# Kernel tuning notes

Hardware: AMD Instinct MI355X
Metric: run time of the kernel (lower is better)

## Reference

```python
import jax, jax.numpy as jnp
import numpy as np

HEAD_DIM = 128
NUM_Q_HEAD = 32
NUM_KV_HEAD = 8
GROUP_SIZE = 128
EPS = 1e-5
WINDOW = 512
CAP = 50.0
CLIP_L, CLIP_R = -0.01, 1.01
SCALE = 1.0 / np.sqrt(HEAD_DIM)
NEG = -1e9


def group_rmsnorm(x, gamma, gsz, eps):
    # x: [B, S, H]; per-group RMS over contiguous chunks of size gsz, then learned scale
    b, s, h = x.shape
    xg = x.reshape(b, s, h // gsz, gsz)
    rms = jnp.sqrt(jnp.mean(xg * xg, axis=-1, keepdims=True) + eps)
    return (xg / rms).reshape(b, s, h) * gamma


def setup_inputs() -> dict:
    key = jax.random.key(0)
    k1, k2, k3, k4, k5 = jax.random.split(key, 5)
    B, S = 2, 2048
    q = jax.random.normal(k1, (B, S, NUM_Q_HEAD, HEAD_DIM), dtype=jnp.float32)
    k = jax.random.normal(k2, (B, S, NUM_KV_HEAD, HEAD_DIM), dtype=jnp.float32)
    v = jax.random.normal(k3, (B, S, NUM_KV_HEAD, HEAD_DIM), dtype=jnp.float32)
    # GroupRMSNorm weights ~ U(init_range) = U(-1, 1)
    gamma_q = jax.random.uniform(k4, (NUM_Q_HEAD * HEAD_DIM,), dtype=jnp.float32, minval=-1.0, maxval=1.0)
    gamma_k = jax.random.uniform(k5, (NUM_KV_HEAD * HEAD_DIM,), dtype=jnp.float32, minval=-1.0, maxval=1.0)
    return {"q": q, "k": k, "v": v, "gamma_q": gamma_q, "gamma_k": gamma_k}


def reference(q, k, v, gamma_q, gamma_k):
    B, Sq, Hq, D = q.shape
    Sk, Hkv = k.shape[1], k.shape[2]
    # QK GroupRMSNorm on flattened hidden dim
    qn = group_rmsnorm(q.reshape(B, Sq, Hq * D), gamma_q, GROUP_SIZE, EPS).reshape(B, Sq, Hq, D)
    kn = group_rmsnorm(k.reshape(B, Sk, Hkv * D), gamma_k, GROUP_SIZE, EPS).reshape(B, Sk, Hkv, D)
    # GQA: repeat_interleave kv heads to match q heads
    rep = Hq // Hkv
    kr = jnp.repeat(kn, rep, axis=2)
    vr = jnp.repeat(v, rep, axis=2)
    # scores: [B, H, Sq, Sk]
    logits = jnp.einsum('bqhd,bkhd->bhqk', qn, kr) * SCALE
    # softmax capping (temperature path skipped when cap is set)
    logits = jnp.tanh(logits / CAP) * CAP
    # causal + sliding-window mask (aligned at sequence end)
    i = jnp.arange(Sq)[:, None]
    j = jnp.arange(Sk)[None, :]
    pos = i + (Sk - Sq)
    allowed = (j <= pos) & (pos - j <= WINDOW)
    logits = jnp.where(allowed, logits, NEG)
    probs = jax.nn.softmax(logits.astype(jnp.float32), axis=-1)
    # softmax clipping: clamp(probs * (r - l) + l, 0, 1)
    probs = jnp.clip(probs * (CLIP_R - CLIP_L) + CLIP_L, 0.0, 1.0)
    # output: [B, Sq, H, D]
    o = jnp.einsum('bhqk,bkhd->bqhd', probs.astype(q.dtype), vr)
    return o
```

## Files before the change

### kernel.cpp

```cpp
#include <hip/hip_runtime.h>

#define SEQ     2048
#define NQH     32
#define NKV     8
#define HD      128
#define WINDOW  512
#define QT      64
#define EPS_F   1e-5f
#define CQ2     0.12752981793f
#define PSTR    72

#define KN_OFF  0ull
#define VT_OFF  8388608ull

#define ROWPAT(r, hg) ((((r) & 3) + 8 * ((r) >> 2)) + 4 * (hg))

#define ASYNC_BAR() asm volatile("s_waitcnt vmcnt(0)\n\ts_barrier" ::: "memory")
#define LGKM_BAR()  asm volatile("s_waitcnt lgkmcnt(0)\n\ts_barrier" ::: "memory")

using bf16x8 = __attribute__((ext_vector_type(8))) __bf16;
using f32x16 = __attribute__((ext_vector_type(16))) float;

__device__ __forceinline__ void dma16(const void* g, void* l) {
    __builtin_amdgcn_global_load_lds(
        (const __attribute__((address_space(1))) unsigned int*)g,
        (__attribute__((address_space(3))) unsigned int*)l, 16, 0, 0);
}

__global__ __launch_bounds__(256)
void prep(const float* __restrict__ k, const float* __restrict__ v,
          const float* __restrict__ gk,
          __bf16* __restrict__ kn, __bf16* __restrict__ vt)
{
    __shared__ __align__(16) __bf16 sT[HD * 72];
    const int blk = blockIdx.x;
    const int tid = threadIdx.x;
    if (blk < 512) {
        const int l16  = tid & 15;
        const int rsub = tid >> 4;
        #pragma unroll
        for (int it = 0; it < 4; it++) {
            const int row = blk * 64 + it * 16 + rsub;
            const float* src = k + (size_t)row * HD + l16 * 8;
            const float* g   = gk + (row & 7) * HD + l16 * 8;
            float4 a  = *(const float4*)(src);
            float4 b4 = *(const float4*)(src + 4);
            float ss = a.x*a.x + a.y*a.y + a.z*a.z + a.w*a.w
                     + b4.x*b4.x + b4.y*b4.y + b4.z*b4.z + b4.w*b4.w;
            ss += __shfl_xor(ss, 1); ss += __shfl_xor(ss, 2);
            ss += __shfl_xor(ss, 4); ss += __shfl_xor(ss, 8);
            const float rs = rsqrtf(ss * (1.f / 128.f) + EPS_F);
            float4 g0 = *(const float4*)(g);
            float4 g1 = *(const float4*)(g + 4);
            bf16x8 o;
            o[0] = (__bf16)(a.x  * rs * g0.x);  o[1] = (__bf16)(a.y  * rs * g0.y);
            o[2] = (__bf16)(a.z  * rs * g0.z);  o[3] = (__bf16)(a.w  * rs * g0.w);
            o[4] = (__bf16)(b4.x * rs * g1.x);  o[5] = (__bf16)(b4.y * rs * g1.y);
            o[6] = (__bf16)(b4.z * rs * g1.z);  o[7] = (__bf16)(b4.w * rs * g1.w);
            *(bf16x8*)(kn + (size_t)row * HD + l16 * 8) = o;
        }
    } else {
        const int blk2 = blk - 512;
        const int st  = blk2 & 31;
        const int kvh = (blk2 >> 5) & 7;
        const int b   = blk2 >> 8;
        const int s0  = st * 64;
        {
            const int r  = tid >> 2;
            const int q4 = tid & 3;
            const float* src = v + ((size_t)(b * SEQ + s0 + r) * NKV + kvh) * HD;
            #pragma unroll
            for (int u = 0; u < 8; u++) {
                const int d0 = q4 * 4 + u * 16;
                float4 x = *(const float4*)(src + d0);
                sT[(d0 + 0) * 72 + r] = (__bf16)x.x;
                sT[(d0 + 1) * 72 + r] = (__bf16)x.y;
                sT[(d0 + 2) * 72 + r] = (__bf16)x.z;
                sT[(d0 + 3) * 72 + r] = (__bf16)x.w;
            }
        }
        __syncthreads();
        {
            const int c     = tid & 7;
            const int dbase = tid >> 3;
            __bf16* dst = vt + ((size_t)(b * NKV + kvh) * HD) * SEQ + s0;
            #pragma unroll
            for (int i = 0; i < 4; i++) {
                const int d = dbase + i * 32;
                bf16x8 w = *(const bf16x8*)&sT[d * 72 + c * 8];
                *(bf16x8*)(dst + (size_t)d * SEQ + c * 8) = w;
            }
        }
    }
}

__global__ __launch_bounds__(256, 2)
void swa_main(const float* __restrict__ q, const __bf16* __restrict__ kn,
              const __bf16* __restrict__ vt, const float* __restrict__ gq,
              float* __restrict__ out)
{
    __shared__ __align__(16) __bf16 sKV[2][QT * HD];
    __shared__ __align__(16) __bf16 sP[QT * PSTR];
    __shared__ float sLp[2][QT];
    __shared__ float sInvL[QT];

    const int wg   = blockIdx.x;
    const int qt   = wg & 31;
    const int h    = (wg >> 5) & 31;
    const int b    = wg >> 10;
    const int kvh  = h >> 2;
    const int i0   = qt * QT;
    const int tid  = threadIdx.x;
    const int lane = tid & 63;
    const int wave = tid >> 6;
    const int mhalf = wave & 1;
    const int nhalf = wave >> 1;
    const int m    = lane & 31;
    const int hg   = lane >> 5;

    const char* k_src[4];  const char* v_src[4];
    int kq_off[4];  int v_off[4];
    {
        const char* kn_head = (const char*)kn + ((size_t)b * SEQ * NKV + kvh) * 256;
        const char* vt_head = (const char*)vt + ((size_t)(b * NKV + kvh) * HD) * (SEQ * 2);
        #pragma unroll
        for (int i = 0; i < 4; i++) {
            const int chunk = wave * 4 + i;
            {
                const int r    = chunk * 4 + (lane >> 4);
                const int cpos = lane & 15;
                const int c    = (cpos & 8) | ((cpos ^ r) & 7);
                k_src[i]  = kn_head + (size_t)r * (NKV * HD * 2) + c * 16;
                kq_off[i] = chunk * 1024;
            }
            {
                const int r    = chunk * 8 + (lane >> 3);
                const int cpos = lane & 7;
                const int c    = cpos ^ (r & 7);
                v_src[i] = vt_head + (size_t)r * (SEQ * 2) + c * 16;
                v_off[i] = chunk * 1024;
            }
        }
    }

    const int t_lo   = (i0 >= WINDOW ? (i0 - WINDOW) : 0) >> 6;
    const int t_hi   = i0 >> 6;
    const int ttbias = t_hi - 8;
    const int krow   = nhalf * 32 + m;

    {
        const size_t ko = (size_t)t_lo * 64 * (NKV * HD * 2);
        const int p0 = (t_lo - ttbias) & 1;
        #pragma unroll
        for (int i = 0; i < 4; i++) dma16(k_src[i] + ko, (char*)&sKV[p0][0] + kq_off[i]);
    }

    bf16x8 qf[8];
    {
        const int qrow = i0 + mhalf * 32 + m;
        const float* qp = q + ((size_t)(b * SEQ + qrow) * NQH + h) * HD;
        float4 qb[16];
        float ss = 0.0f;
        #pragma unroll
        for (int kf = 0; kf < 8; kf++) {
            const int d0 = kf * 16 + hg * 8;
            float4 a  = *(const float4*)(qp + d0);
            float4 b4 = *(const float4*)(qp + d0 + 4);
            qb[kf * 2] = a; qb[kf * 2 + 1] = b4;
            ss += a.x*a.x + a.y*a.y + a.z*a.z + a.w*a.w
                + b4.x*b4.x + b4.y*b4.y + b4.z*b4.z + b4.w*b4.w;
        }
        ss += __shfl_xor(ss, 32);
        const float rs = rsqrtf(ss * (1.f / 128.f) + EPS_F) * CQ2;
        const float* gp = gq + h * HD;
        #pragma unroll
        for (int kf = 0; kf < 8; kf++) {
            const int d0 = kf * 16 + hg * 8;
            float4 g0 = *(const float4*)(gp + d0);
            float4 g1 = *(const float4*)(gp + d0 + 4);
            bf16x8 f;
            f[0] = (__bf16)(qb[kf*2].x   * rs * g0.x);
            f[1] = (__bf16)(qb[kf*2].y   * rs * g0.y);
            f[2] = (__bf16)(qb[kf*2].z   * rs * g0.z);
            f[3] = (__bf16)(qb[kf*2].w   * rs * g0.w);
            f[4] = (__bf16)(qb[kf*2+1].x * rs * g1.x);
            f[5] = (__bf16)(qb[kf*2+1].y * rs * g1.y);
            f[6] = (__bf16)(qb[kf*2+1].z * rs * g1.z);
            f[7] = (__bf16)(qb[kf*2+1].w * rs * g1.w);
            qf[kf] = f;
        }
    }

    float lacc[16];
    #pragma unroll
    for (int i = 0; i < 16; i++) lacc[i] = 0.f;
    bf16x8 ec[9][2];

    #pragma unroll
    for (int tt = 0; tt < 9; tt++) {
        const int t = ttbias + tt;
        if (t >= t_lo) {
            ASYNC_BAR();
            const __bf16* kb = &sKV[tt & 1][0];
            bf16x8 bk[8];
            #pragma unroll
            for (int kf = 0; kf < 8; kf++) {
                const int cc  = kf * 2 + hg;
                const int pos = (cc & 8) | ((cc ^ krow) & 7);
                bk[kf] = *(const bf16x8*)(kb + krow * HD + pos * 8);
            }
            if (t < t_hi) {
                const size_t ko = (size_t)(t + 1) * 64 * (NKV * HD * 2);
                #pragma unroll
                for (int i = 0; i < 4; i++)
                    dma16(k_src[i] + ko, (char*)&sKV[(tt + 1) & 1][0] + kq_off[i]);
            }
            f32x16 c;
            #pragma unroll
            for (int i = 0; i < 16; i++) c[i] = 0.f;
            #pragma unroll
            for (int kf = 0; kf < 8; kf++)
                c = __builtin_amdgcn_mfma_f32_32x32x16_bf16(qf[kf], bk[kf], c, 0, 0, 0);

            const bool do_mask = (t == t_hi) || (t == t_lo && i0 >= WINDOW);
            const int kj = t * 64 + krow;
            float e[16];
            #pragma unroll
            for (int r = 0; r < 16; r++) {
                float ev = __builtin_amdgcn_exp2f(c[r]);
                if (do_mask) {
                    const int qi = i0 + mhalf * 32 + ROWPAT(r, hg);
                    ev = ((unsigned)(qi - kj) <= WINDOW) ? ev : 0.f;
                }
                lacc[r] += ev;
                e[r] = ev;
            }
            bf16x8 p0v, p1v;
            #pragma unroll
            for (int j = 0; j < 8; j++) { p0v[j] = (__bf16)e[j]; p1v[j] = (__bf16)e[8 + j]; }
            ec[tt][0] = p0v;  ec[tt][1] = p1v;
        }
    }

    #pragma unroll
    for (int r = 0; r < 16; r++) {
        float l = lacc[r];
        l += __shfl_xor(l, 1);  l += __shfl_xor(l, 2);  l += __shfl_xor(l, 4);
        l += __shfl_xor(l, 8);  l += __shfl_xor(l, 16);
        lacc[r] = l;
    }
    if (m == 0) {
        #pragma unroll
        for (int r = 0; r < 16; r++)
            sLp[nhalf][mhalf * 32 + ROWPAT(r, hg)] = lacc[r];
    }
    __syncthreads();
    if (tid < QT) sInvL[tid] = __builtin_amdgcn_rcpf(sLp[0][tid] + sLp[1][tid]);
    __syncthreads();

    float ar[16];
    #pragma unroll
    for (int r = 0; r < 16; r++) ar[r] = 1.02f * sInvL[mhalf * 32 + ROWPAT(r, hg)];

    {
        const size_t vo = (size_t)t_lo * 128;
        const int p0 = (t_lo - ttbias) & 1;
        #pragma unroll
        for (int i = 0; i < 4; i++) dma16(v_src[i] + vo, (char*)&sKV[p0][0] + v_off[i]);
    }

    f32x16 o0, o1;
    #pragma unroll
    for (int i = 0; i < 16; i++) { o0[i] = 0.f; o1[i] = 0.f; }

    #pragma unroll
    for (int tt = 0; tt < 9; tt++) {
        const int t = ttbias + tt;
        if (t >= t_lo) {
            ASYNC_BAR();
            #pragma unroll
            for (int half = 0; half < 2; half++) {
                #pragma unroll
                for (int j = 0; j < 8; j++) {
                    const int r = half * 8 + j;
                    const float ee = (float)ec[tt][half][j];
                    const float f = fminf(fmaxf(fmaf(ee, ar[r], -0.01f), 0.f), 1.f);
                    sP[(mhalf * 32 + ROWPAT(r, hg)) * PSTR + krow] = (__bf16)f;
                }
            }
            LGKM_BAR();
            const __bf16* vb = &sKV[tt & 1][0];
            bf16x8 pa[4], vf0[4], vf1[4];
            #pragma unroll
            for (int kf = 0; kf < 4; kf++) {
                pa[kf] = *(const bf16x8*)&sP[(mhalf * 32 + m) * PSTR + kf * 16 + hg * 8];
                const int cc = kf * 2 + hg;
                const int row0 = nhalf * 64 + m;
                const int row1 = nhalf * 64 + 32 + m;
                vf0[kf] = *(const bf16x8*)(vb + row0 * 64 + ((cc ^ row0) & 7) * 8);
                vf1[kf] = *(const bf16x8*)(vb + row1 * 64 + ((cc ^ row1) & 7) * 8);
            }
            if (t < t_hi) {
                const size_t vo = (size_t)(t + 1) * 128;
                #pragma unroll
                for (int i = 0; i < 4; i++)
                    dma16(v_src[i] + vo, (char*)&sKV[(tt + 1) & 1][0] + v_off[i]);
            }
            #pragma unroll
            for (int kf = 0; kf < 4; kf++) {
                o0 = __builtin_amdgcn_mfma_f32_32x32x16_bf16(pa[kf], vf0[kf], o0, 0, 0, 0);
                o1 = __builtin_amdgcn_mfma_f32_32x32x16_bf16(pa[kf], vf1[kf], o1, 0, 0, 0);
            }
        }
    }

    #pragma unroll
    for (int r = 0; r < 16; r++) {
        const int row = i0 + mhalf * 32 + ROWPAT(r, hg);
        float* op = out + ((size_t)(b * SEQ + row) * NQH + h) * HD + nhalf * 64 + m;
        op[0]  = o0[r];
        op[32] = o1[r];
    }
}

extern "C" void kernel_launch(void* const* d_in, const int* in_sizes, int n_in,
                              void* d_out, int out_size, void* d_ws, size_t ws_size,
                              hipStream_t stream) {
    const float* q  = (const float*)d_in[0];
    const float* k  = (const float*)d_in[1];
    const float* v  = (const float*)d_in[2];
    const float* gq = (const float*)d_in[3];
    const float* gk = (const float*)d_in[4];
    float* out = (float*)d_out;

    __bf16* kn = (__bf16*)((char*)d_ws + KN_OFF);
    __bf16* vt = (__bf16*)((char*)d_ws + VT_OFF);

    prep<<<1024, 256, 0, stream>>>(k, v, gk, kn, vt);
    swa_main<<<2 * NQH * (SEQ / QT), 256, 0, stream>>>(q, kn, vt, gq, out);
}
```

Measured before the change: 219.4 us.

## Share K/V tiles across GQA head group with register-staged prefetch

The attention kernel now processes all four query heads of a KV head in one 512-thread workgroup, so each K/V tile is loaded into LDS once and reused by four heads instead of being reloaded per head. The async global-to-LDS DMA is replaced with register-staged prefetch two tiles ahead. The second pass recomputes QK scores rather than caching exponentials in registers. Each wave now owns 32 rows across the full head dimension, which removes the cross-wave row-sum reduction through shared memory. The V transpose in prep is also reworked to use vector LDS writes. In exchange it uses more registers and LDS (64KB), duplicates the QK MFMA work, and adds extra barriers.

```diff
diff --git a/kernel.cpp b/kernel.cpp
--- a/kernel.cpp
+++ b/kernel.cpp
@@ -8,31 +8,23 @@
 #define QT      64
 #define EPS_F   1e-5f
 #define CQ2     0.12752981793f
-#define PSTR    72
 
 #define KN_OFF  0ull
 #define VT_OFF  8388608ull
 
 #define ROWPAT(r, hg) ((((r) & 3) + 8 * ((r) >> 2)) + 4 * (hg))
 
-#define ASYNC_BAR() asm volatile("s_waitcnt vmcnt(0)\n\ts_barrier" ::: "memory")
 #define LGKM_BAR()  asm volatile("s_waitcnt lgkmcnt(0)\n\ts_barrier" ::: "memory")
 
 using bf16x8 = __attribute__((ext_vector_type(8))) __bf16;
 using f32x16 = __attribute__((ext_vector_type(16))) float;
-
-__device__ __forceinline__ void dma16(const void* g, void* l) {
-    __builtin_amdgcn_global_load_lds(
-        (const __attribute__((address_space(1))) unsigned int*)g,
-        (__attribute__((address_space(3))) unsigned int*)l, 16, 0, 0);
-}
 
 __global__ __launch_bounds__(256)
 void prep(const float* __restrict__ k, const float* __restrict__ v,
           const float* __restrict__ gk,
           __bf16* __restrict__ kn, __bf16* __restrict__ vt)
 {
-    __shared__ __align__(16) __bf16 sT[HD * 72];
+    __shared__ __align__(16) __bf16 sT[64 * 136];
     const int blk = blockIdx.x;
     const int tid = threadIdx.x;
     if (blk < 512) {
@@ -66,98 +58,196 @@
         const int b   = blk2 >> 8;
         const int s0  = st * 64;
         {
-            const int r  = tid >> 2;
-            const int q4 = tid & 3;
-            const float* src = v + ((size_t)(b * SEQ + s0 + r) * NKV + kvh) * HD;
+            const int r = tid >> 2, seg = (tid & 3) * 32;
+            const float* src = v + ((size_t)(b * SEQ + s0 + r) * NKV + kvh) * HD + seg;
             #pragma unroll
-            for (int u = 0; u < 8; u++) {
-                const int d0 = q4 * 4 + u * 16;
-                float4 x = *(const float4*)(src + d0);
-                sT[(d0 + 0) * 72 + r] = (__bf16)x.x;
-                sT[(d0 + 1) * 72 + r] = (__bf16)x.y;
-                sT[(d0 + 2) * 72 + r] = (__bf16)x.z;
-                sT[(d0 + 3) * 72 + r] = (__bf16)x.w;
+            for (int u = 0; u < 4; u++) {
+                float4 x = *(const float4*)(src + u * 8);
+                float4 y = *(const float4*)(src + u * 8 + 4);
+                bf16x8 w;
+                w[0] = (__bf16)x.x; w[1] = (__bf16)x.y; w[2] = (__bf16)x.z; w[3] = (__bf16)x.w;
+                w[4] = (__bf16)y.x; w[5] = (__bf16)y.y; w[6] = (__bf16)y.z; w[7] = (__bf16)y.w;
+                *(bf16x8*)&sT[r * 136 + seg + u * 8] = w;
             }
         }
         __syncthreads();
-        {
-            const int c     = tid & 7;
-            const int dbase = tid >> 3;
-            __bf16* dst = vt + ((size_t)(b * NKV + kvh) * HD) * SEQ + s0;
+        __bf16* vtb = vt + (size_t)(b * NKV + kvh) * HD * SEQ;
+        #pragma unroll
+        for (int it = 0; it < 4; it++) {
+            const int id   = tid + it * 256;
+            const int d    = id >> 3;
+            const int sblk = id & 7;
+            bf16x8 w;
             #pragma unroll
-            for (int i = 0; i < 4; i++) {
-                const int d = dbase + i * 32;
-                bf16x8 w = *(const bf16x8*)&sT[d * 72 + c * 8];
-                *(bf16x8*)(dst + (size_t)d * SEQ + c * 8) = w;
+            for (int i = 0; i < 8; i++) {
+                const int j = i ^ sblk;
+                w[j] = sT[(sblk * 8 + j) * 136 + d];
             }
+            *(bf16x8*)(vtb + (size_t)d * SEQ + s0 + sblk * 8) = w;
         }
     }
 }
 
-__global__ __launch_bounds__(256, 2)
+
+#define L1_ITER(T, RDP, LDK0, LDK1, WK0, WK1)                                           \
+  {                                                                                     \
+    const char* kb = smem + (RDP) * 16384;                                              \
+    bf16x8 bk0[8], bk1[8];                                                              \
+    _Pragma("unroll")                                                                   \
+    for (int kf = 0; kf < 8; kf++) {                                                    \
+      const int cc = kf * 2 + hg;                                                       \
+      bk0[kf] = *(const bf16x8*)(kb + m * 256 + (((cc & 8) | ((cc ^ m) & 7)) * 16));    \
+      const int r1 = 32 + m;                                                            \
+      bk1[kf] = *(const bf16x8*)(kb + r1 * 256 + (((cc & 8) | ((cc ^ r1) & 7)) * 16));  \
+    }                                                                                   \
+    { const int tc = ((T) + 2 > t_hi) ? t_hi : (T) + 2;                                 \
+      const char* pp = kgp + (size_t)tc * 131072;                                       \
+      LDK0 = *(const int4*)pp;  LDK1 = *(const int4*)(pp + 16); }                       \
+    { char* dst = smem + (1 - (RDP)) * 16384;                                           \
+      *(int4*)(dst + kds0) = WK0;  *(int4*)(dst + kds1) = WK1; }                        \
+    f32x16 c0, c1;                                                                      \
+    _Pragma("unroll")                                                                   \
+    for (int i = 0; i < 16; i++) { c0[i] = 0.f; c1[i] = 0.f; }                          \
+    _Pragma("unroll")                                                                   \
+    for (int kf = 0; kf < 8; kf++) {                                                    \
+      c0 = __builtin_amdgcn_mfma_f32_32x32x16_bf16(qf[kf], bk0[kf], c0, 0, 0, 0);       \
+      c1 = __builtin_amdgcn_mfma_f32_32x32x16_bf16(qf[kf], bk1[kf], c1, 0, 0, 0);       \
+    }                                                                                   \
+    const bool do_mask = ((T) == t_hi) || ((T) == t_lo && i0 >= WINDOW);                \
+    const int kj0 = (T) * 64 + m;                                                       \
+    _Pragma("unroll")                                                                   \
+    for (int r = 0; r < 16; r++) {                                                      \
+      const int qi = i0 + sub * 32 + ROWPAT(r, hg);                                     \
+      float e0 = __builtin_amdgcn_exp2f(c0[r]);                                         \
+      float e1 = __builtin_amdgcn_exp2f(c1[r]);                                         \
+      if (do_mask) {                                                                    \
+        e0 = ((unsigned)(qi - kj0) <= WINDOW) ? e0 : 0.f;                               \
+        e1 = ((unsigned)(qi - kj0 - 32) <= WINDOW) ? e1 : 0.f;                          \
+      }                                                                                 \
+      lacc[r] += e0 + e1;                                                               \
+    }                                                                                   \
+    LGKM_BAR();                                                                         \
+  }
+
+#define L2_ITER(T, LDK0, LDK1, LDV0, LDV1, WK0, WK1, WV0, WV1)                          \
+  {                                                                                     \
+    bf16x8 bk0[8], bk1[8];                                                              \
+    _Pragma("unroll")                                                                   \
+    for (int kf = 0; kf < 8; kf++) {                                                    \
+      const int cc = kf * 2 + hg;                                                       \
+      bk0[kf] = *(const bf16x8*)(smem + m * 256 + (((cc & 8) | ((cc ^ m) & 7)) * 16));  \
+      const int r1 = 32 + m;                                                            \
+      bk1[kf] = *(const bf16x8*)(smem + r1 * 256 + (((cc & 8) | ((cc ^ r1) & 7)) * 16));\
+    }                                                                                   \
+    { const int tc = ((T) + 2 > t_hi) ? t_hi : (T) + 2;                                 \
+      const char* pk = kgp + (size_t)tc * 131072;                                       \
+      const char* pv = vgp + (size_t)tc * 128;                                          \
+      LDK0 = *(const int4*)pk;  LDK1 = *(const int4*)(pk + 16);                         \
+      LDV0 = *(const int4*)pv;  LDV1 = *(const int4*)(pv + 16); }                       \
+    f32x16 c0, c1;                                                                      \
+    _Pragma("unroll")                                                                   \
+    for (int i = 0; i < 16; i++) { c0[i] = 0.f; c1[i] = 0.f; }                          \
+    _Pragma("unroll")                                                                   \
+    for (int kf = 0; kf < 8; kf++) {                                                    \
+      c0 = __builtin_amdgcn_mfma_f32_32x32x16_bf16(qf[kf], bk0[kf], c0, 0, 0, 0);       \
+      c1 = __builtin_amdgcn_mfma_f32_32x32x16_bf16(qf[kf], bk1[kf], c1, 0, 0, 0);       \
+    }                                                                                   \
+    const bool do_mask = ((T) == t_hi) || ((T) == t_lo && i0 >= WINDOW);                \
+    const int kj0 = (T) * 64 + m;                                                       \
+    _Pragma("unroll")                                                                   \
+    for (int r = 0; r < 16; r++) {                                                      \
+      const int rowr = sub * 32 + ROWPAT(r, hg);                                        \
+      const int qi = i0 + rowr;                                                         \
+      float e0 = __builtin_amdgcn_exp2f(c0[r]);                                         \
+      float e1 = __builtin_amdgcn_exp2f(c1[r]);                                         \
+      if (do_mask) {                                                                    \
+        e0 = ((unsigned)(qi - kj0) <= WINDOW) ? e0 : 0.f;                               \
+        e1 = ((unsigned)(qi - kj0 - 32) <= WINDOW) ? e1 : 0.f;                          \
+      }                                                                                 \
+      const float f0 = fminf(fmaxf(fmaf(e0, ar[r], -0.01f), 0.f), 1.f);                 \
+      const float f1 = fminf(fmaxf(fmaf(e1, ar[r], -0.01f), 0.f), 1.f);                 \
+      *(__bf16*)(smem + 32768 + hh * 8192 + rowr * 128                                  \
+                 + ((((m >> 3) ^ (rowr & 7)) * 8 + (m & 7)) * 2)) = (__bf16)f0;         \
+      *(__bf16*)(smem + 32768 + hh * 8192 + rowr * 128                                  \
+                 + (((((m + 32) >> 3) ^ (rowr & 7)) * 8 + (m & 7)) * 2)) = (__bf16)f1;  \
+    }                                                                                   \
+    LGKM_BAR();                     \
+    *(int4*)(smem + kds0) = WK0;  *(int4*)(smem + kds1) = WK1;    \
+    {                                                                                   \
+      bf16x8 pa[4];                                                                     \
+      const int rw = sub * 32 + m;                                                      \
+      _Pragma("unroll")                                                                 \
+      for (int kf = 0; kf < 4; kf++) {                                                  \
+        const int cc = kf * 2 + hg;                                                     \
+        pa[kf] = *(const bf16x8*)(smem + 32768 + hh * 8192 + rw * 128                   \
+                                  + ((cc ^ (rw & 7)) * 16));                            \
+      }                                                                                 \
+      _Pragma("unroll")                                                                 \
+      for (int nb = 0; nb < 4; nb++) {                                                  \
+        const int d = nb * 32 + m;                                                      \
+        _Pragma("unroll")                                                               \
+        for (int kf = 0; kf < 4; kf++) {                                                \
+          const int cc = kf * 2 + hg;                                                   \
+          bf16x8 vf = *(const bf16x8*)(smem + 16384 + d * 128 + ((cc ^ (d & 7)) * 16)); \
+          o[nb] = __builtin_amdgcn_mfma_f32_32x32x16_bf16(pa[kf], vf, o[nb], 0, 0, 0);  \
+        }                                                                               \
+      }                                                                                 \
+    }                                                                                   \
+    LGKM_BAR();                                      \
+    *(int4*)(smem + vds0) = WV0;  *(int4*)(smem + vds1) = WV1;    \
+  }
+
+__global__ __launch_bounds__(512, 2)
 void swa_main(const float* __restrict__ q, const __bf16* __restrict__ kn,
               const __bf16* __restrict__ vt, const float* __restrict__ gq,
               float* __restrict__ out)
 {
-    __shared__ __align__(16) __bf16 sKV[2][QT * HD];
-    __shared__ __align__(16) __bf16 sP[QT * PSTR];
-    __shared__ float sLp[2][QT];
-    __shared__ float sInvL[QT];
+    __shared__ __align__(16) char smem[65536];
 
     const int wg   = blockIdx.x;
     const int qt   = wg & 31;
-    const int h    = (wg >> 5) & 31;
-    const int b    = wg >> 10;
-    const int kvh  = h >> 2;
+    const int kvh  = (wg >> 5) & 7;
+    const int b    = wg >> 8;
     const int i0   = qt * QT;
     const int tid  = threadIdx.x;
+    const int wave = tid >> 6;
+    const int hh   = wave >> 1;
+    const int sub  = wave & 1;
+    const int h    = kvh * 4 + hh;
     const int lane = tid & 63;
-    const int wave = tid >> 6;
-    const int mhalf = wave & 1;
-    const int nhalf = wave >> 1;
     const int m    = lane & 31;
     const int hg   = lane >> 5;
 
-    const char* k_src[4];  const char* v_src[4];
-    int kq_off[4];  int v_off[4];
+    const int krw = tid >> 3;
+    const int kc  = (tid & 7) * 2;
+    const char* kgp = (const char*)kn + ((size_t)b * SEQ * NKV + kvh) * 256
+                      + (size_t)krw * 2048 + (tid & 7) * 32;
+    const int kds0 = krw * 256 + (((kc & 8) | ((kc ^ krw) & 7)) * 16);
+    const int kds1 = kds0 ^ 16;
+
+    const int vrw = tid >> 2;
+    const int vc  = (tid & 3) * 2;
+    const char* vgp = (const char*)vt + ((size_t)(b * NKV + kvh) * HD + vrw) * (SEQ * 2)
+                      + (tid & 3) * 32;
+    const int vds0 = 16384 + vrw * 128 + ((vc ^ (vrw & 7)) * 16);
+    const int vds1 = vds0 ^ 16;
+
+    const int t_lo = (i0 >= WINDOW ? (i0 - WINDOW) : 0) >> 6;
+    const int t_hi = i0 >> 6;
+
+    int4 stgA0, stgA1, stgB0, stgB1;
     {
-        const char* kn_head = (const char*)kn + ((size_t)b * SEQ * NKV + kvh) * 256;
-        const char* vt_head = (const char*)vt + ((size_t)(b * NKV + kvh) * HD) * (SEQ * 2);
-        #pragma unroll
-        for (int i = 0; i < 4; i++) {
-            const int chunk = wave * 4 + i;
-            {
-                const int r    = chunk * 4 + (lane >> 4);
-                const int cpos = lane & 15;
-                const int c    = (cpos & 8) | ((cpos ^ r) & 7);
-                k_src[i]  = kn_head + (size_t)r * (NKV * HD * 2) + c * 16;
-                kq_off[i] = chunk * 1024;
-            }
-            {
-                const int r    = chunk * 8 + (lane >> 3);
-                const int cpos = lane & 7;
-                const int c    = cpos ^ (r & 7);
-                v_src[i] = vt_head + (size_t)r * (SEQ * 2) + c * 16;
-                v_off[i] = chunk * 1024;
-            }
-        }
-    }
-
-    const int t_lo   = (i0 >= WINDOW ? (i0 - WINDOW) : 0) >> 6;
-    const int t_hi   = i0 >> 6;
-    const int ttbias = t_hi - 8;
-    const int krow   = nhalf * 32 + m;
-
-    {
-        const size_t ko = (size_t)t_lo * 64 * (NKV * HD * 2);
-        const int p0 = (t_lo - ttbias) & 1;
-        #pragma unroll
-        for (int i = 0; i < 4; i++) dma16(k_src[i] + ko, (char*)&sKV[p0][0] + kq_off[i]);
+        const char* p0 = kgp + (size_t)t_lo * 131072;
+        stgA0 = *(const int4*)p0;  stgA1 = *(const int4*)(p0 + 16);
+        const int t1 = (t_lo + 1 > t_hi) ? t_hi : t_lo + 1;
+        const char* p1 = kgp + (size_t)t1 * 131072;
+        stgB0 = *(const int4*)p1;  stgB1 = *(const int4*)(p1 + 16);
+        *(int4*)(smem + kds0) = stgA0;  *(int4*)(smem + kds1) = stgA1;
     }
 
     bf16x8 qf[8];
     {
-        const int qrow = i0 + mhalf * 32 + m;
+        const int qrow = i0 + sub * 32 + m;
         const float* qp = q + ((size_t)(b * SEQ + qrow) * NQH + h) * HD;
         float4 qb[16];
         float ss = 0.0f;
@@ -190,136 +280,63 @@
             qf[kf] = f;
         }
     }
+    LGKM_BAR();
 
     float lacc[16];
     #pragma unroll
     for (int i = 0; i < 16; i++) lacc[i] = 0.f;
-    bf16x8 ec[9][2];
-
-    #pragma unroll
-    for (int tt = 0; tt < 9; tt++) {
-        const int t = ttbias + tt;
-        if (t >= t_lo) {
-            ASYNC_BAR();
-            const __bf16* kb = &sKV[tt & 1][0];
-            bf16x8 bk[8];
-            #pragma unroll
-            for (int kf = 0; kf < 8; kf++) {
-                const int cc  = kf * 2 + hg;
-                const int pos = (cc & 8) | ((cc ^ krow) & 7);
-                bk[kf] = *(const bf16x8*)(kb + krow * HD + pos * 8);
-            }
-            if (t < t_hi) {
-                const size_t ko = (size_t)(t + 1) * 64 * (NKV * HD * 2);
-                #pragma unroll
-                for (int i = 0; i < 4; i++)
-                    dma16(k_src[i] + ko, (char*)&sKV[(tt + 1) & 1][0] + kq_off[i]);
-            }
-            f32x16 c;
-            #pragma unroll
-            for (int i = 0; i < 16; i++) c[i] = 0.f;
-            #pragma unroll
-            for (int kf = 0; kf < 8; kf++)
-                c = __builtin_amdgcn_mfma_f32_32x32x16_bf16(qf[kf], bk[kf], c, 0, 0, 0);
-
-            const bool do_mask = (t == t_hi) || (t == t_lo && i0 >= WINDOW);
-            const int kj = t * 64 + krow;
-            float e[16];
-            #pragma unroll
-            for (int r = 0; r < 16; r++) {
-                float ev = __builtin_amdgcn_exp2f(c[r]);
-                if (do_mask) {
-                    const int qi = i0 + mhalf * 32 + ROWPAT(r, hg);
-                    ev = ((unsigned)(qi - kj) <= WINDOW) ? ev : 0.f;
-                }
-                lacc[r] += ev;
-                e[r] = ev;
-            }
-            bf16x8 p0v, p1v;
-            #pragma unroll
-            for (int j = 0; j < 8; j++) { p0v[j] = (__bf16)e[j]; p1v[j] = (__bf16)e[8 + j]; }
-            ec[tt][0] = p0v;  ec[tt][1] = p1v;
-        }
-    }
-
+
+    for (int t = t_lo; t <= t_hi; t += 2) {
+        L1_ITER(t, 0, stgA0, stgA1, stgB0, stgB1);
+        if (t + 1 <= t_hi) { L1_ITER(t + 1, 1, stgB0, stgB1, stgA0, stgA1); }
+    }
+
+    float ar[16];
     #pragma unroll
     for (int r = 0; r < 16; r++) {
         float l = lacc[r];
         l += __shfl_xor(l, 1);  l += __shfl_xor(l, 2);  l += __shfl_xor(l, 4);
         l += __shfl_xor(l, 8);  l += __shfl_xor(l, 16);
-        lacc[r] = l;
-    }
-    if (m == 0) {
-        #pragma unroll
-        for (int r = 0; r < 16; r++)
-            sLp[nhalf][mhalf * 32 + ROWPAT(r, hg)] = lacc[r];
-    }
-    __syncthreads();
-    if (tid < QT) sInvL[tid] = __builtin_amdgcn_rcpf(sLp[0][tid] + sLp[1][tid]);
-    __syncthreads();
-
-    float ar[16];
+        ar[r] = 1.02f * __builtin_amdgcn_rcpf(l);
+    }
+
+    int4 skA0, skA1, svA0, svA1, skB0, skB1, svB0, svB1;
+    {
+        const char* pk = kgp + (size_t)t_lo * 131072;
+        const char* pv = vgp + (size_t)t_lo * 128;
+        skA0 = *(const int4*)pk;  skA1 = *(const int4*)(pk + 16);
+        svA0 = *(const int4*)pv;  svA1 = *(const int4*)(pv + 16);
+        const int t1 = (t_lo + 1 > t_hi) ? t_hi : t_lo + 1;
+        const char* pk1 = kgp + (size_t)t1 * 131072;
+        const char* pv1 = vgp + (size_t)t1 * 128;
+        skB0 = *(const int4*)pk1;  skB1 = *(const int4*)(pk1 + 16);
+        svB0 = *(const int4*)pv1;  svB1 = *(const int4*)(pv1 + 16);
+        *(int4*)(smem + kds0) = skA0;  *(int4*)(smem + kds1) = skA1;
+        *(int4*)(smem + vds0) = svA0;  *(int4*)(smem + vds1) = svA1;
+    }
+    LGKM_BAR();
+
+    f32x16 o[4];
     #pragma unroll
-    for (int r = 0; r < 16; r++) ar[r] = 1.02f * sInvL[mhalf * 32 + ROWPAT(r, hg)];
-
-    {
-        const size_t vo = (size_t)t_lo * 128;
-        const int p0 = (t_lo - ttbias) & 1;
-        #pragma unroll
-        for (int i = 0; i < 4; i++) dma16(v_src[i] + vo, (char*)&sKV[p0][0] + v_off[i]);
-    }
-
-    f32x16 o0, o1;
-    #pragma unroll
-    for (int i = 0; i < 16; i++) { o0[i] = 0.f; o1[i] = 0.f; }
-
-    #pragma unroll
-    for (int tt = 0; tt < 9; tt++) {
-        const int t = ttbias + tt;
-        if (t >= t_lo) {
-            ASYNC_BAR();
-            #pragma unroll
-            for (int half = 0; half < 2; half++) {
-                #pragma unroll
-                for (int j = 0; j < 8; j++) {
-                    const int r = half * 8 + j;
-                    const float ee = (float)ec[tt][half][j];
-                    const float f = fminf(fmaxf(fmaf(ee, ar[r], -0.01f), 0.f), 1.f);
-                    sP[(mhalf * 32 + ROWPAT(r, hg)) * PSTR + krow] = (__bf16)f;
-                }
-            }
-            LGKM_BAR();
-            const __bf16* vb = &sKV[tt & 1][0];
-            bf16x8 pa[4], vf0[4], vf1[4];
-            #pragma unroll
-            for (int kf = 0; kf < 4; kf++) {
-                pa[kf] = *(const bf16x8*)&sP[(mhalf * 32 + m) * PSTR + kf * 16 + hg * 8];
-                const int cc = kf * 2 + hg;
-                const int row0 = nhalf * 64 + m;
-                const int row1 = nhalf * 64 + 32 + m;
-                vf0[kf] = *(const bf16x8*)(vb + row0 * 64 + ((cc ^ row0) & 7) * 8);
-                vf1[kf] = *(const bf16x8*)(vb + row1 * 64 + ((cc ^ row1) & 7) * 8);
-            }
-            if (t < t_hi) {
-                const size_t vo = (size_t)(t + 1) * 128;
-                #pragma unroll
-                for (int i = 0; i < 4; i++)
-                    dma16(v_src[i] + vo, (char*)&sKV[(tt + 1) & 1][0] + v_off[i]);
-            }
-            #pragma unroll
-            for (int kf = 0; kf < 4; kf++) {
-                o0 = __builtin_amdgcn_mfma_f32_32x32x16_bf16(pa[kf], vf0[kf], o0, 0, 0, 0);
-                o1 = __builtin_amdgcn_mfma_f32_32x32x16_bf16(pa[kf], vf1[kf], o1, 0, 0, 0);
-            }
+    for (int nb = 0; nb < 4; nb++)
+        #pragma unroll
+        for (int i = 0; i < 16; i++) o[nb][i] = 0.f;
+
+    for (int t = t_lo; t <= t_hi; t += 2) {
+        L2_ITER(t, skA0, skA1, svA0, svA1, skB0, skB1, svB0, svB1);
+        if (t + 1 <= t_hi) {
+            L2_ITER(t + 1, skB0, skB1, svB0, svB1, skA0, skA1, svA0, svA1);
         }
     }
 
     #pragma unroll
     for (int r = 0; r < 16; r++) {
-        const int row = i0 + mhalf * 32 + ROWPAT(r, hg);
-        float* op = out + ((size_t)(b * SEQ + row) * NQH + h) * HD + nhalf * 64 + m;
-        op[0]  = o0[r];
-        op[32] = o1[r];
+        const int row = i0 + sub * 32 + ROWPAT(r, hg);
+        float* op = out + ((size_t)(b * SEQ + row) * NQH + h) * HD + m;
+        op[0]  = o[0][r];
+        op[32] = o[1][r];
+        op[64] = o[2][r];
+        op[96] = o[3][r];
     }
 }
 
@@ -337,5 +354,5 @@
     __bf16* vt = (__bf16*)((char*)d_ws + VT_OFF);
 
     prep<<<1024, 256, 0, stream>>>(k, v, gk, kn, vt);
-    swa_main<<<2 * NQH * (SEQ / QT), 256, 0, stream>>>(q, kn, vt, gq, out);
+    swa_main<<<2 * NKV * (SEQ / QT), 512, 0, stream>>>(q, kn, vt, gq, out);
 }
```

Result: slower. 229.5 us (+4.6%).
